# Kernel optimization log

Measured on AMD Instinct MI355X. Metric: run time of the kernel, lower is better.

Reference implementation:

```python
import jax, jax.numpy as jnp
from jax import lax
import numpy as np
import math

INPUT_DIM = 64
HIDDEN_DIM = 512
SEQ_LEN = 256
BATCH = 512
PRED_LEN = 24
NUM_TARGETS = 1


def setup_inputs() -> dict:
    key = jax.random.key(0)
    ks = jax.random.split(key, 10)
    stdv = 1.0 / math.sqrt(HIDDEN_DIM)
    u = lambda k, shape: jax.random.uniform(k, shape, jnp.float32, -stdv, stdv)
    return {
        "x": jax.random.normal(ks[0], (BATCH, SEQ_LEN, INPUT_DIM), jnp.float32),
        "Wa": u(ks[1], (INPUT_DIM, INPUT_DIM)),
        "Ua": u(ks[2], (2 * HIDDEN_DIM, INPUT_DIM)),
        "ba": jnp.zeros((INPUT_DIM,), jnp.float32),
        "Va": u(ks[3], (INPUT_DIM, INPUT_DIM)),
        "W_ih": u(ks[4], (4 * HIDDEN_DIM, INPUT_DIM)),
        "W_hh": u(ks[5], (4 * HIDDEN_DIM, HIDDEN_DIM)),
        "b_ih": u(ks[6], (4 * HIDDEN_DIM,)),
        "b_hh": u(ks[7], (4 * HIDDEN_DIM,)),
        "fc_w": u(ks[8], (PRED_LEN * NUM_TARGETS, HIDDEN_DIM)),
        "fc_b": u(ks[9], (PRED_LEN * NUM_TARGETS,)),
    }


def reference(x, Wa, Ua, ba, Va, W_ih, W_hh, b_ih, b_hh, fc_w, fc_b):
    B, S, D = x.shape
    H = W_hh.shape[1]

    def step(carry, x_t):
        h, c = carry  # [B,H] each
        # attention gate over input features
        hc = jnp.concatenate([h, c], axis=1)  # [B,2H]
        a_t = jnp.tanh(x_t @ Wa + hc @ Ua + ba) @ Va  # [B,D]
        alpha_t = jax.nn.softmax(a_t, axis=1)
        x_att = alpha_t * x_t
        # torch.nn.LSTMCell: gates in order i, f, g, o
        gates = x_att @ W_ih.T + h @ W_hh.T + b_ih + b_hh  # [B,4H]
        i, f, g, o = jnp.split(gates, 4, axis=1)
        c_new = jax.nn.sigmoid(f) * c + jax.nn.sigmoid(i) * jnp.tanh(g)
        h_new = jax.nn.sigmoid(o) * jnp.tanh(c_new)
        return (h_new, c_new), None

    h0 = jnp.zeros((B, H), x.dtype)
    c0 = jnp.zeros((B, H), x.dtype)
    (h_T, _), _ = lax.scan(step, (h0, c0), jnp.swapaxes(x, 0, 1))  # scan over seq
    y = h_T @ fc_w.T + fc_b  # [B, pred_len*num_targets]
    return y.reshape(B, PRED_LEN, NUM_TARGETS)
```

## Files before the change

### kernel.cpp

```cpp
#include <hip/hip_runtime.h>
#include <math.h>

#define B 512
#define S 256
#define D 64
#define H 512
#define BH (B*H)
#define KSTEPS 8

#define HBUF_OFF 0
#define CBUF_OFF (2*BH)
#define XATT_OFF (3*BH)
#define FLAGS_OFF (3*BH + B*D)
#define NFLAGS 1024

#define WAIT_VM0 asm volatile("s_waitcnt vmcnt(0)" ::: "memory")

__device__ __forceinline__ void ldg_sc(float4& r, const float* p) {
    asm volatile("global_load_dwordx4 %0, %1, off sc0 sc1" : "=v"(r) : "v"(p));
}
__device__ __forceinline__ void st_sc(float* p, float v) {
    asm volatile("global_store_dword %0, %1, off sc0 sc1" :: "v"(p), "v"(v));
}
__device__ __forceinline__ void waitf(unsigned int* f, unsigned int tgt) {
    if (threadIdx.x == 0) {
        unsigned int spin = 0;
        while (__hip_atomic_load(f, __ATOMIC_RELAXED, __HIP_MEMORY_SCOPE_AGENT) < tgt) {
            __builtin_amdgcn_s_sleep(2);
            if (++spin > (1u << 18)) break;
        }
    }
    __syncthreads();
}
__device__ __forceinline__ void bumpf(unsigned int* f) {
    __hip_atomic_fetch_add(f, 1u, __ATOMIC_RELAXED, __HIP_MEMORY_SCOPE_AGENT);
}

__global__ __launch_bounds__(256) void init_zero(float* __restrict__ ws) {
    int i = blockIdx.x * blockDim.x + threadIdx.x;
    if (i < BH) {
        ws[HBUF_OFF + i] = 0.f;
        ws[CBUF_OFF + i] = 0.f;
    }
    if (i < NFLAGS) ((unsigned int*)(ws + FLAGS_OFF))[i] = 0u;
}

__global__ __launch_bounds__(256, 2) void fused_kernel(
    const float* __restrict__ x, const float* __restrict__ Wa,
    const float* __restrict__ Ua, const float* __restrict__ ba,
    const float* __restrict__ Va,
    const float* __restrict__ Wih, const float* __restrict__ Whh,
    const float* __restrict__ bih, const float* __restrict__ bhh,
    float* __restrict__ ws, int base)
{
    const int bid = blockIdx.x;
    const int tid = threadIdx.x;
    float* h32 = ws + HBUF_OFF;
    float* c32 = ws + CBUF_OFF;
    float* xatt = ws + XATT_OFF;
    unsigned int* flags = (unsigned int*)(ws + FLAGS_OFF);

    __shared__ float h_lds[32][68];
    __shared__ float w_lds[4][32][68];
    __shared__ float c_t[32][36];
    __shared__ float h2[2][512];
    __shared__ float c2[2][512];
    __shared__ float part[2][2][64];
    __shared__ float ta[2][64];
    __shared__ float pv[2][2][64];

    if (bid < 256) {
        const int d = tid & 63;
        const int rr = (tid >> 6) & 1;
        const int p = tid >> 7;
        const int r_t = bid >> 4;
        const int brow = bid * 2 + rr;
        unsigned int* hf = flags + r_t * 32;
        unsigned int* xf = flags + 512 + r_t * 32;

        for (int sub = 0; sub < KSTEPS; ++sub) {
            const int ts = base + sub;
            const int rd = ts & 1;
            waitf(hf, 16u * (unsigned int)ts);

            {
                float4 hv, cv;
                const int row = bid * 2 + (tid >> 7);
                ldg_sc(hv, h32 + (size_t)rd * BH + (size_t)row * H + (tid & 127) * 4);
                ldg_sc(cv, c32 + (size_t)row * H + (tid & 127) * 4);
                WAIT_VM0;
                *(float4*)&h2[tid >> 7][(tid & 127) * 4] = hv;
                *(float4*)&c2[tid >> 7][(tid & 127) * 4] = cv;
            }
            __syncthreads();

            const float* __restrict__ xrow = x + ((size_t)brow * S + ts) * D;
            float a = 0.f;
            if (p == 0) {
                a = ba[d];
                #pragma unroll 8
                for (int k = 0; k < D; ++k) a += xrow[k] * Wa[k*D + d];
                #pragma unroll 8
                for (int k = 0; k < H; ++k) a += h2[rr][k] * Ua[k*D + d];
            } else {
                #pragma unroll 8
                for (int k = 0; k < H; ++k) a += c2[rr][k] * Ua[(size_t)(H + k)*D + d];
            }
            part[rr][p][d] = a;
            __syncthreads();
            if (p == 0) ta[rr][d] = tanhf(part[rr][0][d] + part[rr][1][d]);
            __syncthreads();
            float av = 0.f;
            {
                const int k0 = p * 32;
                #pragma unroll 8
                for (int k = k0; k < k0 + 32; ++k) av += ta[rr][k] * Va[k*D + d];
            }
            pv[rr][p][d] = av;
            __syncthreads();
            float v = pv[rr][0][d] + pv[rr][1][d];
            float m = v;
            #pragma unroll
            for (int o = 32; o > 0; o >>= 1) m = fmaxf(m, __shfl_xor(m, o));
            float e = expf(v - m);
            float ssum = e;
            #pragma unroll
            for (int o = 32; o > 0; o >>= 1) ssum += __shfl_xor(ssum, o);
            if (p == 0) {
                st_sc(xatt + (size_t)brow * D + d, (e / ssum) * xrow[d]);
            }
            WAIT_VM0;
            __syncthreads();
            if (tid == 0) bumpf(xf);
        }
    } else {
        const int g = bid - 256;
        const int u_t = g & 15, r_t = g >> 4;
        const int u0 = u_t * 32, r0 = r_t * 32;
        const int tm = tid & 7, tn = tid >> 3;
        const int u = u0 + tn;
        unsigned int* hf = flags + r_t * 32;
        unsigned int* xf = flags + 512 + r_t * 32;

        const float bs0 = bih[0*H + u] + bhh[0*H + u];
        const float bs1 = bih[1*H + u] + bhh[1*H + u];
        const float bs2 = bih[2*H + u] + bhh[2*H + u];
        const float bs3 = bih[3*H + u] + bhh[3*H + u];

        for (int sub = 0; sub < KSTEPS; ++sub) {
            const int ts = base + sub;
            const int rd = ts & 1, wrs = rd ^ 1;
            waitf(hf, 16u * (unsigned int)ts);

            float acc[4][4];
            #pragma unroll
            for (int i = 0; i < 4; ++i)
                #pragma unroll
                for (int q = 0; q < 4; ++q) acc[i][q] = 0.f;

            for (int kb = 0; kb < 9; ++kb) {
                if (kb == 8) waitf(xf, 16u * (unsigned int)(ts + 1));
                __syncthreads();
                {
                    const float* src; int ldsrc, kofs;
                    if (kb < 8) { src = Whh; ldsrc = H; kofs = kb*64; }
                    else        { src = Wih; ldsrc = D; kofs = 0; }
                    #pragma unroll
                    for (int it = 0; it < 8; ++it) {
                        int j = tid + it*256;
                        int f4c = j & 15, row = j >> 4;
                        int uu = row & 31, q = row >> 5;
                        float4 v = *(const float4*)(src + (size_t)(q*H + u0 + uu)*ldsrc + kofs + f4c*4);
                        *(float4*)&w_lds[q][uu][f4c*4] = v;
                    }
                    float4 a0, a1, ctv;
                    {
                        int j0 = tid, j1 = tid + 256;
                        int f0 = j0 & 15, rl0 = j0 >> 4;
                        int f1 = j1 & 15, rl1 = j1 >> 4;
                        if (kb < 8) {
                            const float* hb = h32 + (size_t)rd * BH;
                            ldg_sc(a0, hb + (size_t)(r0 + rl0)*H + kb*64 + f0*4);
                            ldg_sc(a1, hb + (size_t)(r0 + rl1)*H + kb*64 + f1*4);
                        } else {
                            ldg_sc(a0, xatt + (size_t)(r0 + rl0)*D + f0*4);
                            ldg_sc(a1, xatt + (size_t)(r0 + rl1)*D + f1*4);
                        }
                        if (kb == 0)
                            ldg_sc(ctv, c32 + (size_t)(r0 + (tid >> 3))*H + u0 + (tid & 7)*4);
                        WAIT_VM0;
                        *(float4*)&h_lds[rl0][f0*4] = a0;
                        *(float4*)&h_lds[rl1][f1*4] = a1;
                        if (kb == 0)
                            *(float4*)&c_t[tid >> 3][(tid & 7)*4] = ctv;
                    }
                }
                __syncthreads();
                #pragma unroll
                for (int k4 = 0; k4 < 16; ++k4) {
                    float4 wv[4], hv[4];
                    #pragma unroll
                    for (int q = 0; q < 4; ++q)
                        wv[q] = *(const float4*)&w_lds[q][tn][k4*4];
                    #pragma unroll
                    for (int i = 0; i < 4; ++i)
                        hv[i] = *(const float4*)&h_lds[tm + 8*i][k4*4];
                    #pragma unroll
                    for (int i = 0; i < 4; ++i)
                        #pragma unroll
                        for (int q = 0; q < 4; ++q) {
                            acc[i][q] = fmaf(hv[i].x, wv[q].x, acc[i][q]);
                            acc[i][q] = fmaf(hv[i].y, wv[q].y, acc[i][q]);
                            acc[i][q] = fmaf(hv[i].z, wv[q].z, acc[i][q]);
                            acc[i][q] = fmaf(hv[i].w, wv[q].w, acc[i][q]);
                        }
                }
            }

            float* __restrict__ hW = h32 + (size_t)wrs * BH;
            #pragma unroll
            for (int i = 0; i < 4; ++i) {
                const int b = r0 + tm + 8*i;
                float gi = acc[i][0] + bs0;
                float gf = acc[i][1] + bs1;
                float gg = acc[i][2] + bs2;
                float go = acc[i][3] + bs3;
                float c_old = c_t[tm + 8*i][tn];
                float si = 1.f / (1.f + expf(-gi));
                float sf = 1.f / (1.f + expf(-gf));
                float so = 1.f / (1.f + expf(-go));
                float cn = sf * c_old + si * tanhf(gg);
                float hn = so * tanhf(cn);
                st_sc(c32 + (size_t)b * H + u, cn);
                st_sc(hW + (size_t)b * H + u, hn);
            }
            WAIT_VM0;
            __syncthreads();
            if (tid == 0) bumpf(hf);
        }
    }
}

__global__ __launch_bounds__(256) void fc_kernel(
    const float* __restrict__ fcw, const float* __restrict__ fcb,
    const float* __restrict__ ws, float* __restrict__ out)
{
    const int b = blockIdx.x;
    __shared__ float hrow[H];
    const float* __restrict__ hp = ws + HBUF_OFF + (size_t)b*H;
    for (int k = threadIdx.x; k < H; k += 256) hrow[k] = hp[k];
    __syncthreads();
    int j = threadIdx.x;
    if (j < 24) {
        float a = fcb[j];
        #pragma unroll 8
        for (int k = 0; k < H; ++k) a += hrow[k] * fcw[j*H + k];
        out[b*24 + j] = a;
    }
}

extern "C" void kernel_launch(void* const* d_in, const int* in_sizes, int n_in,
                              void* d_out, int out_size, void* d_ws, size_t ws_size,
                              hipStream_t stream) {
    const float* x   = (const float*)d_in[0];
    const float* Wa  = (const float*)d_in[1];
    const float* Ua  = (const float*)d_in[2];
    const float* ba  = (const float*)d_in[3];
    const float* Va  = (const float*)d_in[4];
    const float* Wih = (const float*)d_in[5];
    const float* Whh = (const float*)d_in[6];
    const float* bih = (const float*)d_in[7];
    const float* bhh = (const float*)d_in[8];
    const float* fcw = (const float*)d_in[9];
    const float* fcb = (const float*)d_in[10];
    float* out = (float*)d_out;
    float* ws  = (float*)d_ws;

    hipLaunchKernelGGL(init_zero, dim3((BH + 255)/256), dim3(256), 0, stream, ws);
    for (int base = 0; base < S; base += KSTEPS) {
        hipLaunchKernelGGL(fused_kernel, dim3(512), dim3(256), 0, stream,
                           x, Wa, Ua, ba, Va, Wih, Whh, bih, bhh, ws, base);
    }
    hipLaunchKernelGGL(fc_kernel, dim3(B), dim3(256), 0, stream, fcw, fcb, ws, out);
}
```

Baseline: 8.656 ms.

## Prefetch next hidden-state chunk during FMA loop and interleave attention/LSTM blocks

The LSTM gate blocks now issue the global loads for the next 64-column chunk of h right after the barrier, so those loads overlap the current chunk's FMA loop. A double-buffered h_act LDS array holds the two chunks. Attention and LSTM work are also interleaved by block-ID parity instead of split into two contiguous halves, which changes how the two roles are spread over CUs. This adds LDS usage and register pressure, and the prefetched loads rely on the vmcnt wait that precedes the next LDS store.

Result: slower. 10.81 ms (+24.9%).

```diff
diff --git a/kernel.cpp b/kernel.cpp
--- a/kernel.cpp
+++ b/kernel.cpp
@@ -60,7 +60,7 @@
     float* xatt = ws + XATT_OFF;
     unsigned int* flags = (unsigned int*)(ws + FLAGS_OFF);
 
-    __shared__ float h_lds[32][68];
+    __shared__ float h_act[2][32][68];
     __shared__ float w_lds[4][32][68];
     __shared__ float c_t[32][36];
     __shared__ float h2[2][512];
@@ -69,12 +69,14 @@
     __shared__ float ta[2][64];
     __shared__ float pv[2][2][64];
 
-    if (bid < 256) {
+    const int id = bid >> 1;
+
+    if ((bid & 1) == 0) {
         const int d = tid & 63;
         const int rr = (tid >> 6) & 1;
         const int p = tid >> 7;
-        const int r_t = bid >> 4;
-        const int brow = bid * 2 + rr;
+        const int r_t = id >> 4;
+        const int brow = id * 2 + rr;
         unsigned int* hf = flags + r_t * 32;
         unsigned int* xf = flags + 512 + r_t * 32;
 
@@ -85,7 +87,7 @@
 
             {
                 float4 hv, cv;
-                const int row = bid * 2 + (tid >> 7);
+                const int row = id * 2 + (tid >> 7);
                 ldg_sc(hv, h32 + (size_t)rd * BH + (size_t)row * H + (tid & 127) * 4);
                 ldg_sc(cv, c32 + (size_t)row * H + (tid & 127) * 4);
                 WAIT_VM0;
@@ -134,7 +136,7 @@
             if (tid == 0) bumpf(xf);
         }
     } else {
-        const int g = bid - 256;
+        const int g = id;
         const int u_t = g & 15, r_t = g >> 4;
         const int u0 = u_t * 32, r0 = r_t * 32;
         const int tm = tid & 7, tn = tid >> 3;
@@ -147,6 +149,9 @@
         const float bs2 = bih[2*H + u] + bhh[2*H + u];
         const float bs3 = bih[3*H + u] + bhh[3*H + u];
 
+        const int f0 = tid & 15, rl0 = tid >> 4;
+        const int f1 = (tid + 256) & 15, rl1 = (tid + 256) >> 4;
+
         for (int sub = 0; sub < KSTEPS; ++sub) {
             const int ts = base + sub;
             const int rd = ts & 1, wrs = rd ^ 1;
@@ -158,8 +163,15 @@
                 #pragma unroll
                 for (int q = 0; q < 4; ++q) acc[i][q] = 0.f;
 
+            float4 pa0, pa1, ctv;
+            {
+                const float* hb = h32 + (size_t)rd * BH;
+                ldg_sc(pa0, hb + (size_t)(r0 + rl0)*H + f0*4);
+                ldg_sc(pa1, hb + (size_t)(r0 + rl1)*H + f1*4);
+                ldg_sc(ctv, c32 + (size_t)(r0 + (tid >> 3))*H + u0 + (tid & 7)*4);
+            }
+
             for (int kb = 0; kb < 9; ++kb) {
-                if (kb == 8) waitf(xf, 16u * (unsigned int)(ts + 1));
                 __syncthreads();
                 {
                     const float* src; int ldsrc, kofs;
@@ -173,29 +185,24 @@
                         float4 v = *(const float4*)(src + (size_t)(q*H + u0 + uu)*ldsrc + kofs + f4c*4);
                         *(float4*)&w_lds[q][uu][f4c*4] = v;
                     }
-                    float4 a0, a1, ctv;
-                    {
-                        int j0 = tid, j1 = tid + 256;
-                        int f0 = j0 & 15, rl0 = j0 >> 4;
-                        int f1 = j1 & 15, rl1 = j1 >> 4;
-                        if (kb < 8) {
-                            const float* hb = h32 + (size_t)rd * BH;
-                            ldg_sc(a0, hb + (size_t)(r0 + rl0)*H + kb*64 + f0*4);
-                            ldg_sc(a1, hb + (size_t)(r0 + rl1)*H + kb*64 + f1*4);
-                        } else {
-                            ldg_sc(a0, xatt + (size_t)(r0 + rl0)*D + f0*4);
-                            ldg_sc(a1, xatt + (size_t)(r0 + rl1)*D + f1*4);
-                        }
-                        if (kb == 0)
-                            ldg_sc(ctv, c32 + (size_t)(r0 + (tid >> 3))*H + u0 + (tid & 7)*4);
-                        WAIT_VM0;
-                        *(float4*)&h_lds[rl0][f0*4] = a0;
-                        *(float4*)&h_lds[rl1][f1*4] = a1;
-                        if (kb == 0)
-                            *(float4*)&c_t[tid >> 3][(tid & 7)*4] = ctv;
-                    }
-                }
+                }
+                if (kb == 8) {
+                    waitf(xf, 16u * (unsigned int)(ts + 1));
+                    ldg_sc(pa0, xatt + (size_t)(r0 + rl0)*D + f0*4);
+                    ldg_sc(pa1, xatt + (size_t)(r0 + rl1)*D + f1*4);
+                }
+                WAIT_VM0;
+                *(float4*)&h_act[kb & 1][rl0][f0*4] = pa0;
+                *(float4*)&h_act[kb & 1][rl1][f1*4] = pa1;
+                if (kb == 0)
+                    *(float4*)&c_t[tid >> 3][(tid & 7)*4] = ctv;
                 __syncthreads();
+                if (kb < 7) {
+                    const float* hb = h32 + (size_t)rd * BH;
+                    ldg_sc(pa0, hb + (size_t)(r0 + rl0)*H + (kb + 1)*64 + f0*4);
+                    ldg_sc(pa1, hb + (size_t)(r0 + rl1)*H + (kb + 1)*64 + f1*4);
+                }
+                const int cb = kb & 1;
                 #pragma unroll
                 for (int k4 = 0; k4 < 16; ++k4) {
                     float4 wv[4], hv[4];
@@ -204,7 +211,7 @@
                         wv[q] = *(const float4*)&w_lds[q][tn][k4*4];
                     #pragma unroll
                     for (int i = 0; i < 4; ++i)
-                        hv[i] = *(const float4*)&h_lds[tm + 8*i][k4*4];
+                        hv[i] = *(const float4*)&h_act[cb][tm + 8*i][k4*4];
                     #pragma unroll
                     for (int i = 0; i < 4; ++i)
                         #pragma unroll
```
